# Kernel optimization log

Measured on AMD Instinct MI355X. Metric: run time of the kernel, lower is better.

The kernel has to match this reference:

```python
import jax, jax.numpy as jnp
import numpy as np

B, N, D, H = 4, 4096, 1024, 16
HD = D // H  # 64
EPS_NORM = 1e-12  # F.normalize eps
EPS_LN = 1e-5     # layernorm eps


def setup_inputs() -> dict:
    key = jax.random.key(0)
    ks = jax.random.split(key, 9)
    s = 0.02
    return {
        "x": jax.random.normal(ks[0], (B, N, D), jnp.float32),
        "Wq": jax.random.normal(ks[1], (D, D), jnp.float32) * s,
        "Wk": jax.random.normal(ks[2], (D, D), jnp.float32) * s,
        "Wv": jax.random.normal(ks[3], (D, D), jnp.float32) * s,
        "Wf": jax.random.normal(ks[4], (H, D), jnp.float32) * s,
        "Wg1": jax.random.normal(ks[5], (HD, D), jnp.float32) * s,
        "Wg2": jax.random.normal(ks[6], (D, HD), jnp.float32) * s,
        "ln_w": jnp.ones((D,), jnp.float32),
        "Wo": jax.random.normal(ks[7], (D, D), jnp.float32) * s,
    }


def _silu(x):
    return x * jax.nn.sigmoid(x)


def _simple_gla(q, k, v, f):
    # q,k,v: [B,N,H,HD], f: [B,N,H] log-decay. Recurrence:
    #   S_t = exp(f_t) * S_{t-1} + k_t v_t^T ;  o_t = q_t^T S_t  (scale=1)
    qT = jnp.moveaxis(q, 1, 0)  # [N,B,H,HD]
    kT = jnp.moveaxis(k, 1, 0)
    vT = jnp.moveaxis(v, 1, 0)
    fT = jnp.moveaxis(f, 1, 0)  # [N,B,H]

    def step(S, inp):
        qt, kt, vt, ft = inp
        S = jnp.exp(ft)[..., None, None] * S + kt[..., :, None] * vt[..., None, :]
        o = jnp.einsum('bhk,bhkv->bhv', qt, S)
        return S, o

    S0 = jnp.zeros((q.shape[0], q.shape[2], q.shape[3], v.shape[3]), q.dtype)
    _, o = jax.lax.scan(step, S0, (qT, kT, vT, fT))
    return jnp.moveaxis(o, 0, 1)  # [B,N,H,HD]


def reference(x, Wq, Wk, Wv, Wf, Wg1, Wg2, ln_w, Wo):
    b, n, d = x.shape
    q = _silu(x @ Wq.T).reshape(b, n, H, HD)
    k = _silu(x @ Wk.T).reshape(b, n, H, HD)
    v = _silu(x @ Wv.T).reshape(b, n, H, HD)
    f = jax.nn.log_sigmoid(x @ Wf.T)  # [B,N,H] scalar per-head log decay
    # F.normalize(k, p=2, dim=-1)
    k = k / jnp.maximum(jnp.linalg.norm(k, axis=-1, keepdims=True), EPS_NORM)

    o = _simple_gla(q, k, v, f).reshape(b, n, d)

    # output gate: sigmoid(Linear(d->hd) -> Linear(hd->d))
    gate = jax.nn.sigmoid((x @ Wg1.T) @ Wg2.T)
    o = o * gate

    # layernorm without bias
    mu = jnp.mean(o, axis=-1, keepdims=True)
    xc = o - mu
    var = jnp.mean(xc * xc, axis=-1, keepdims=True)
    o = xc / jnp.sqrt(var + EPS_LN) * ln_w

    return o @ Wo.T
```

## Files before the change

### kernel.cpp

```cpp
#include <hip/hip_runtime.h>
#include <stdint.h>


#define NWIDE 3200

typedef __attribute__((ext_vector_type(4))) float f32x4;
typedef __attribute__((ext_vector_type(4))) unsigned short u16x4;
typedef __attribute__((ext_vector_type(8))) unsigned short u16x8;
typedef __attribute__((ext_vector_type(8))) __bf16 bf16x8;

__device__ __forceinline__ float bf2f(unsigned short u) {
    union { unsigned int i; float f; } c; c.i = ((unsigned int)u) << 16; return c.f;
}
__device__ __forceinline__ unsigned short f2bf(float f) {
    union { float f; unsigned int i; } c; c.f = f;
    return (unsigned short)((c.i + 0x7fffu + ((c.i >> 16) & 1u)) >> 16);
}
__device__ __forceinline__ f32x4 MFMA(bf16x8 a, bf16x8 b, f32x4 c) {
    return __builtin_amdgcn_mfma_f32_16x16x32_bf16(a, b, c, 0, 0, 0);
}
__device__ __forceinline__ void lds16(const void* g, void* l) {
    __builtin_amdgcn_global_load_lds(
        (const __attribute__((address_space(1))) unsigned int*)(uintptr_t)g,
        (__attribute__((address_space(3))) unsigned int*)(unsigned int)(uintptr_t)l,
        16, 0, 0);
}

__global__ __launch_bounds__(256) void k_convert(const float* __restrict__ src,
                                                 unsigned short* __restrict__ dst, int n4) {
    int i = blockIdx.x * 256 + threadIdx.x;
    if (i >= n4) return;
    f32x4 v = ((const f32x4*)src)[i];
    u16x4 o;
#pragma unroll
    for (int e = 0; e < 4; e++) o[e] = f2bf(v[e]);
    ((u16x4*)dst)[i] = o;
}

__global__ __launch_bounds__(256) void k_wcat(const float* __restrict__ Wq, const float* __restrict__ Wk,
                                              const float* __restrict__ Wv, const float* __restrict__ Wf,
                                              const float* __restrict__ Wg1, unsigned short* __restrict__ Wcat) {
    const int r = blockIdx.x, t = threadIdx.x;
    const float* src = nullptr; int sr = r;
    if (r < 1024) { src = Wq; }
    else if (r < 2048) { src = Wk; sr = r - 1024; }
    else if (r < 3072) { src = Wv; sr = r - 2048; }
    else if (r < 3088) { src = Wf; sr = r - 3072; }
    else if (r < 3152) { src = Wg1; sr = r - 3088; }
    u16x4 o;
    if (src) {
        f32x4 v = *(const f32x4*)&src[(size_t)sr * 1024 + 4 * t];
#pragma unroll
        for (int e = 0; e < 4; e++) o[e] = f2bf(v[e]);
    } else {
        o[0] = 0; o[1] = 0; o[2] = 0; o[3] = 0;
    }
    *(u16x4*)&Wcat[(size_t)r * 1024 + 4 * t] = o;
}

template <int MODE>
__global__ __launch_bounds__(256)
void k_gemm(const unsigned short* __restrict__ A, const unsigned short* __restrict__ Bw,
            void* __restrict__ outp, float* __restrict__ zbuf, int M, int N, int K, int ldOut) {
    __shared__ __align__(16) unsigned short As[128 * 32];
    __shared__ __align__(16) unsigned short Bs[128 * 32];
    const int tid = threadIdx.x;
    const int w = tid >> 6, lane = tid & 63;
    const int m0 = blockIdx.x * 128, n0 = blockIdx.y * 128;
    const int srow = lane >> 2, scol = (lane & 3) * 8;
    const int fr = lane & 15, fg = lane >> 4;
    const int wr = w >> 1, wc = w & 1;
    f32x4 acc[4][4] = {};
    const int kc = K >> 5;
    for (int kt = 0; kt < kc; ++kt) {
        const int k0 = kt << 5;
        __syncthreads();
        {
            const unsigned short* ga = A + (size_t)(m0 + 32 * w + srow) * K + k0 + scol;
            lds16(ga, &As[(32 * w) * 32]);
            const unsigned short* ga2 = A + (size_t)(m0 + 32 * w + 16 + srow) * K + k0 + scol;
            lds16(ga2, &As[(32 * w + 16) * 32]);
            const unsigned short* gb = Bw + (size_t)(n0 + 32 * w + srow) * K + k0 + scol;
            lds16(gb, &Bs[(32 * w) * 32]);
            const unsigned short* gb2 = Bw + (size_t)(n0 + 32 * w + 16 + srow) * K + k0 + scol;
            lds16(gb2, &Bs[(32 * w + 16) * 32]);
        }
        __syncthreads();
        bf16x8 av[4], bv[4];
#pragma unroll
        for (int i = 0; i < 4; i++) av[i] = *(const bf16x8*)&As[(64 * wr + 16 * i + fr) * 32 + fg * 8];
#pragma unroll
        for (int j = 0; j < 4; j++) bv[j] = *(const bf16x8*)&Bs[(64 * wc + 16 * j + fr) * 32 + fg * 8];
#pragma unroll
        for (int i = 0; i < 4; i++)
#pragma unroll
            for (int j = 0; j < 4; j++)
                acc[i][j] = MFMA(av[i], bv[j], acc[i][j]);
    }
#pragma unroll
    for (int i = 0; i < 4; i++)
#pragma unroll
        for (int j = 0; j < 4; j++) {
            const int gc = n0 + 64 * wc + 16 * j + fr;
#pragma unroll
            for (int r = 0; r < 4; r++) {
                const int gr = m0 + 64 * wr + 16 * i + 4 * fg + r;
                float v = acc[i][j][r];
                if (MODE == 0) {
                    ((unsigned short*)outp)[(size_t)gr * ldOut + gc] = f2bf(v);
                    if (gc >= 3072 && gc < 3088) zbuf[gr * 16 + (gc - 3072)] = v;
                } else {
                    ((float*)outp)[(size_t)gr * ldOut + gc] = v;
                }
            }
        }
}

__global__ __launch_bounds__(256)
void k_act(unsigned short* __restrict__ Y, const float* __restrict__ zbuf, float* __restrict__ fbuf) {
    const int r = blockIdx.x, t = threadIdx.x;
    unsigned short* Yr = Y + (size_t)r * NWIDE;
    {
        u16x4 a = *(u16x4*)&Yr[4 * t]; u16x4 o;
#pragma unroll
        for (int e = 0; e < 4; e++) { float x = bf2f(a[e]); o[e] = f2bf(x / (1.f + __expf(-x))); }
        *(u16x4*)&Yr[4 * t] = o;
    }
    {
        u16x4 a = *(u16x4*)&Yr[2048 + 4 * t]; u16x4 o;
#pragma unroll
        for (int e = 0; e < 4; e++) { float x = bf2f(a[e]); o[e] = f2bf(x / (1.f + __expf(-x))); }
        *(u16x4*)&Yr[2048 + 4 * t] = o;
    }
    {
        u16x4 a = *(u16x4*)&Yr[1024 + 4 * t];
        float f[4]; float ssum = 0.f;
#pragma unroll
        for (int e = 0; e < 4; e++) { float x = bf2f(a[e]); f[e] = x / (1.f + __expf(-x)); ssum += f[e] * f[e]; }
#pragma unroll
        for (int m = 1; m < 16; m <<= 1) ssum += __shfl_xor(ssum, m, 16);
        float scale = 1.f / fmaxf(sqrtf(ssum), 1e-12f);
        u16x4 o;
#pragma unroll
        for (int e = 0; e < 4; e++) o[e] = f2bf(f[e] * scale);
        *(u16x4*)&Yr[1024 + 4 * t] = o;
    }
    if (t < 16) {
        float z = zbuf[r * 16 + t];
        float f = (z >= 0.f) ? -log1pf(__expf(-z)) : (z - log1pf(__expf(z)));
        fbuf[r * 16 + t] = f;
    }
}

__global__ void k_cumsum(const float* __restrict__ fbuf, float* __restrict__ cbuf) {
    const int cid = blockIdx.x, t = threadIdx.x;
    const int bh = cid >> 6, ic = cid & 63;
    const int b = bh >> 4, h = bh & 15;
    float v = fbuf[(size_t)(b * 4096 + ic * 64 + t) * 16 + h];
#pragma unroll
    for (int off = 1; off < 64; off <<= 1) {
        float u = __shfl_up(v, (unsigned)off, 64);
        if (t >= off) v += u;
    }
    cbuf[(size_t)cid * 64 + t] = v;
}

__global__ __launch_bounds__(256)
void k_chunk_kv(const unsigned short* __restrict__ Y, const float* __restrict__ cbuf,
                unsigned short* __restrict__ St) {
    __shared__ __align__(16) unsigned short Kt[64 * 72];
    __shared__ __align__(16) unsigned short Vt[64 * 72];
    __shared__ float cs[64];
    const int cid = blockIdx.x, tid = threadIdx.x;
    const int bh = cid >> 6, ic = cid & 63;
    const int b = bh >> 4, h = bh & 15;
    if (tid < 64) cs[tid] = cbuf[(size_t)cid * 64 + tid];
    __syncthreads();
    const int s = tid >> 2, c0 = (tid & 3) << 4;
    const float wdec = __expf(cs[63] - cs[s]);
    const size_t rowg = (size_t)(b * 4096 + ic * 64 + s) * NWIDE;
    u16x8 k0v = *(const u16x8*)&Y[rowg + 1024 + h * 64 + c0];
    u16x8 k1v = *(const u16x8*)&Y[rowg + 1024 + h * 64 + c0 + 8];
    u16x8 v0v = *(const u16x8*)&Y[rowg + 2048 + h * 64 + c0];
    u16x8 v1v = *(const u16x8*)&Y[rowg + 2048 + h * 64 + c0 + 8];
#pragma unroll
    for (int e = 0; e < 8; e++) {
        Kt[(c0 + e) * 72 + s] = f2bf(bf2f(k0v[e]) * wdec);
        Kt[(c0 + 8 + e) * 72 + s] = f2bf(bf2f(k1v[e]) * wdec);
        Vt[(c0 + e) * 72 + s] = v0v[e];
        Vt[(c0 + 8 + e) * 72 + s] = v1v[e];
    }
    __syncthreads();
    const int w = tid >> 6, lane = tid & 63;
    const int fr = lane & 15, fg = lane >> 4;
    f32x4 acc[4] = {};
#pragma unroll
    for (int ks = 0; ks < 2; ks++) {
        bf16x8 a = *(const bf16x8*)&Kt[(16 * w + fr) * 72 + ks * 32 + fg * 8];
#pragma unroll
        for (int j = 0; j < 4; j++)
            acc[j] = MFMA(a, *(const bf16x8*)&Vt[(16 * j + fr) * 72 + ks * 32 + fg * 8], acc[j]);
    }
    unsigned short* outp = St + (size_t)cid * 4096;
#pragma unroll
    for (int j = 0; j < 4; j++)
#pragma unroll
        for (int r = 0; r < 4; r++)
            outp[(16 * w + 4 * fg + r) * 64 + 16 * j + fr] = f2bf(acc[j][r]);
}

__global__ void k_scan(unsigned short* __restrict__ St, const float* __restrict__ cbuf) {
    const int bh = blockIdx.x >> 4;
    const int e = ((blockIdx.x & 15) << 8) + threadIdx.x;
    float S = 0.f;
    const size_t base = (size_t)bh * 64 * 4096 + e;
    for (int i = 0; i < 64; i++) {
        const float d = __expf(cbuf[(bh * 64 + i) * 64 + 63]);
        const float m = bf2f(St[base + (size_t)i * 4096]);
        St[base + (size_t)i * 4096] = f2bf(S);
        S = d * S + m;
    }
}

__global__ __launch_bounds__(256)
void k_chunk_out(const unsigned short* __restrict__ Y, const float* __restrict__ cbuf,
                 const unsigned short* __restrict__ St, const unsigned short* __restrict__ Wg2b,
                 unsigned short* __restrict__ og) {
    __shared__ __align__(16) unsigned short Qs[64 * 72];
    __shared__ __align__(16) unsigned short Ks[64 * 72];
    __shared__ __align__(16) unsigned short Vt[64 * 72];
    __shared__ __align__(16) unsigned short S0[64 * 72];
    __shared__ __align__(16) unsigned short G1[64 * 72];
    __shared__ __align__(16) unsigned short W2[64 * 72];
    __shared__ __align__(16) unsigned short Pl[4 * 16 * 72];
    __shared__ float cs[64];
    const int cid = blockIdx.x, tid = threadIdx.x;
    const int bh = cid >> 6, ic = cid & 63;
    const int b = bh >> 4, h = bh & 15;
    if (tid < 64) cs[tid] = cbuf[(size_t)cid * 64 + tid];
    const int s = tid >> 2, c0 = (tid & 3) << 4;
    const size_t rowg = (size_t)(b * 4096 + ic * 64 + s) * NWIDE;
    *(u16x8*)&Qs[s * 72 + c0] = *(const u16x8*)&Y[rowg + h * 64 + c0];
    *(u16x8*)&Qs[s * 72 + c0 + 8] = *(const u16x8*)&Y[rowg + h * 64 + c0 + 8];
    *(u16x8*)&Ks[s * 72 + c0] = *(const u16x8*)&Y[rowg + 1024 + h * 64 + c0];
    *(u16x8*)&Ks[s * 72 + c0 + 8] = *(const u16x8*)&Y[rowg + 1024 + h * 64 + c0 + 8];
    *(u16x8*)&G1[s * 72 + c0] = *(const u16x8*)&Y[rowg + 3088 + c0];
    *(u16x8*)&G1[s * 72 + c0 + 8] = *(const u16x8*)&Y[rowg + 3088 + c0 + 8];
    *(u16x8*)&W2[s * 72 + c0] = *(const u16x8*)&Wg2b[(size_t)(h * 64 + s) * 64 + c0];
    *(u16x8*)&W2[s * 72 + c0 + 8] = *(const u16x8*)&Wg2b[(size_t)(h * 64 + s) * 64 + c0 + 8];
    {
        u16x8 v0v = *(const u16x8*)&Y[rowg + 2048 + h * 64 + c0];
        u16x8 v1v = *(const u16x8*)&Y[rowg + 2048 + h * 64 + c0 + 8];
        u16x8 s0v = *(const u16x8*)&St[(size_t)cid * 4096 + s * 64 + c0];
        u16x8 s1v = *(const u16x8*)&St[(size_t)cid * 4096 + s * 64 + c0 + 8];
#pragma unroll
        for (int e = 0; e < 8; e++) {
            Vt[(c0 + e) * 72 + s] = v0v[e];
            Vt[(c0 + 8 + e) * 72 + s] = v1v[e];
            S0[(c0 + e) * 72 + s] = s0v[e];
            S0[(c0 + 8 + e) * 72 + s] = s1v[e];
        }
    }
    __syncthreads();
    const int w = tid >> 6, lane = tid & 63;
    const int fr = lane & 15, fg = lane >> 4;
    bf16x8 aq[2];
#pragma unroll
    for (int ks = 0; ks < 2; ks++) aq[ks] = *(const bf16x8*)&Qs[(16 * w + fr) * 72 + ks * 32 + fg * 8];
    f32x4 sc[4] = {};
#pragma unroll
    for (int ks = 0; ks < 2; ks++)
#pragma unroll
        for (int j = 0; j < 4; j++)
            sc[j] = MFMA(aq[ks], *(const bf16x8*)&Ks[(16 * j + fr) * 72 + ks * 32 + fg * 8], sc[j]);
    const int tl = 16 * w + 4 * fg;
#pragma unroll
    for (int j = 0; j < 4; j++)
#pragma unroll
        for (int r = 0; r < 4; r++) {
            const int tt = tl + r, ss2 = 16 * j + fr;
            float p = (ss2 <= tt) ? sc[j][r] * __expf(cs[tt] - cs[ss2]) : 0.f;
            Pl[w * (16 * 72) + (4 * fg + r) * 72 + ss2] = f2bf(p);
        }
    __syncthreads();
    f32x4 ov[4] = {};
#pragma unroll
    for (int ks = 0; ks < 2; ks++) {
        bf16x8 ap = *(const bf16x8*)&Pl[w * (16 * 72) + fr * 72 + ks * 32 + fg * 8];
#pragma unroll
        for (int j = 0; j < 4; j++)
            ov[j] = MFMA(ap, *(const bf16x8*)&Vt[(16 * j + fr) * 72 + ks * 32 + fg * 8], ov[j]);
    }
    f32x4 qs[4] = {};
#pragma unroll
    for (int ks = 0; ks < 2; ks++)
#pragma unroll
        for (int j = 0; j < 4; j++)
            qs[j] = MFMA(aq[ks], *(const bf16x8*)&S0[(16 * j + fr) * 72 + ks * 32 + fg * 8], qs[j]);
    bf16x8 ag[2];
#pragma unroll
    for (int ks = 0; ks < 2; ks++) ag[ks] = *(const bf16x8*)&G1[(16 * w + fr) * 72 + ks * 32 + fg * 8];
    f32x4 gl[4] = {};
#pragma unroll
    for (int ks = 0; ks < 2; ks++)
#pragma unroll
        for (int j = 0; j < 4; j++)
            gl[j] = MFMA(ag[ks], *(const bf16x8*)&W2[(16 * j + fr) * 72 + ks * 32 + fg * 8], gl[j]);
#pragma unroll
    for (int j = 0; j < 4; j++)
#pragma unroll
        for (int r = 0; r < 4; r++) {
            const int tt = tl + r;
            const float o = ov[j][r] + __expf(cs[tt]) * qs[j][r];
            const float g = 1.f / (1.f + __expf(-gl[j][r]));
            og[(size_t)(b * 4096 + ic * 64 + tt) * 1024 + h * 64 + 16 * j + fr] = f2bf(o * g);
        }
}

__global__ __launch_bounds__(256)
void k_ln(unsigned short* __restrict__ og, const float* __restrict__ lnw) {
    __shared__ float red[8];
    const int r = blockIdx.x, t = threadIdx.x;
    unsigned short* p = og + (size_t)r * 1024;
    u16x4 a = *(u16x4*)&p[4 * t];
    float x[4]; float s = 0.f, ssum = 0.f;
#pragma unroll
    for (int e = 0; e < 4; e++) { x[e] = bf2f(a[e]); s += x[e]; ssum += x[e] * x[e]; }
#pragma unroll
    for (int m = 1; m < 64; m <<= 1) { s += __shfl_xor(s, m, 64); ssum += __shfl_xor(ssum, m, 64); }
    const int w = t >> 6;
    if ((t & 63) == 0) { red[w] = s; red[4 + w] = ssum; }
    __syncthreads();
    s = red[0] + red[1] + red[2] + red[3];
    ssum = red[4] + red[5] + red[6] + red[7];
    const float mu = s * (1.f / 1024.f);
    const float var = ssum * (1.f / 1024.f) - mu * mu;
    const float rs = rsqrtf(var + 1e-5f);
    u16x4 o;
#pragma unroll
    for (int e = 0; e < 4; e++) o[e] = f2bf((x[e] - mu) * rs * lnw[4 * t + e]);
    *(u16x4*)&p[4 * t] = o;
}

extern "C" void kernel_launch(void* const* d_in, const int* in_sizes, int n_in,
                              void* d_out, int out_size, void* d_ws, size_t ws_size,
                              hipStream_t stream) {
    const float* x = (const float*)d_in[0];
    const float* Wq = (const float*)d_in[1];
    const float* Wk = (const float*)d_in[2];
    const float* Wv = (const float*)d_in[3];
    const float* Wf = (const float*)d_in[4];
    const float* Wg1 = (const float*)d_in[5];
    const float* Wg2 = (const float*)d_in[6];
    const float* lnw = (const float*)d_in[7];
    const float* Wo = (const float*)d_in[8];
    char* ws = (char*)d_ws;
    unsigned short* xb = (unsigned short*)(ws + 0);
    unsigned short* Yb = (unsigned short*)(ws + 33554432LL);
    unsigned short* Wcat = (unsigned short*)(ws + 138412032LL);
    unsigned short* Wob = (unsigned short*)(ws + 144965632LL);
    unsigned short* Wg2b = (unsigned short*)(ws + 147062784LL);
    float* zbuf = (float*)(ws + 147193856LL);
    float* fbuf = (float*)(ws + 148242432LL);
    float* cbuf = (float*)(ws + 149291008LL);
    unsigned short* St = (unsigned short*)(ws + 150339584LL);
    unsigned short* og = (unsigned short*)(ws + 183894016LL);

    k_convert<<<16384, 256, 0, stream>>>(x, xb, 4194304);
    k_wcat<<<3200, 256, 0, stream>>>(Wq, Wk, Wv, Wf, Wg1, Wcat);
    k_convert<<<1024, 256, 0, stream>>>(Wo, Wob, 262144);
    k_convert<<<64, 256, 0, stream>>>(Wg2, Wg2b, 16384);
    k_gemm<0><<<dim3(128, 25), 256, 0, stream>>>(xb, Wcat, Yb, zbuf, 16384, 3200, 1024, 3200);
    k_act<<<16384, 256, 0, stream>>>(Yb, zbuf, fbuf);
    k_cumsum<<<4096, 64, 0, stream>>>(fbuf, cbuf);
    k_chunk_kv<<<4096, 256, 0, stream>>>(Yb, cbuf, St);
    k_scan<<<1024, 256, 0, stream>>>(St, cbuf);
    k_chunk_out<<<4096, 256, 0, stream>>>(Yb, cbuf, St, Wg2b, og);
    k_ln<<<16384, 256, 0, stream>>>(og, lnw);
    k_gemm<1><<<dim3(128, 8), 256, 0, stream>>>(og, Wob, d_out, nullptr, 16384, 1024, 1024, 1024);
}
```

Before: 364.5 us.

## Replace GEMMs with 256x256 double-buffered swizzled kernel and fuse activations into epilogue

```diff
diff --git a/kernel.cpp b/kernel.cpp
--- a/kernel.cpp
+++ b/kernel.cpp
@@ -15,6 +15,10 @@
 __device__ __forceinline__ unsigned short f2bf(float f) {
     union { float f; unsigned int i; } c; c.f = f;
     return (unsigned short)((c.i + 0x7fffu + ((c.i >> 16) & 1u)) >> 16);
+}
+__device__ __forceinline__ float siluf(float x) { return x / (1.f + __expf(-x)); }
+__device__ __forceinline__ float logsigf(float z) {
+    return (z >= 0.f) ? -log1pf(__expf(-z)) : (z - log1pf(__expf(z)));
 }
 __device__ __forceinline__ f32x4 MFMA(bf16x8 a, bf16x8 b, f32x4 c) {
     return __builtin_amdgcn_mfma_f32_16x16x32_bf16(a, b, c, 0, 0, 0);
@@ -58,97 +62,168 @@
     *(u16x4*)&Wcat[(size_t)r * 1024 + 4 * t] = o;
 }
 
+
+template <int I0>
+__device__ __forceinline__ void mfma16(const bf16x8* av, const bf16x8* bv, f32x4 (&acc)[8][4]) {
+#pragma unroll
+    for (int di = 0; di < 2; di++)
+#pragma unroll
+        for (int j = 0; j < 4; j++)
+#pragma unroll
+            for (int ks = 0; ks < 2; ks++)
+                acc[I0 + di][j] = MFMA(av[di * 2 + ks], bv[j * 2 + ks], acc[I0 + di][j]);
+}
+
 template <int MODE>
-__global__ __launch_bounds__(256)
-void k_gemm(const unsigned short* __restrict__ A, const unsigned short* __restrict__ Bw,
-            void* __restrict__ outp, float* __restrict__ zbuf, int M, int N, int K, int ldOut) {
-    __shared__ __align__(16) unsigned short As[128 * 32];
-    __shared__ __align__(16) unsigned short Bs[128 * 32];
+__global__ __launch_bounds__(512, 2)
+void k_gemm256(const unsigned short* __restrict__ A, const unsigned short* __restrict__ Bw,
+               void* __restrict__ outp, float* __restrict__ fbuf, int NT) {
+    __shared__ __align__(16) char smem[131072];
     const int tid = threadIdx.x;
     const int w = tid >> 6, lane = tid & 63;
-    const int m0 = blockIdx.x * 128, n0 = blockIdx.y * 128;
-    const int srow = lane >> 2, scol = (lane & 3) * 8;
     const int fr = lane & 15, fg = lane >> 4;
-    const int wr = w >> 1, wc = w & 1;
-    f32x4 acc[4][4] = {};
-    const int kc = K >> 5;
-    for (int kt = 0; kt < kc; ++kt) {
-        const int k0 = kt << 5;
-        __syncthreads();
-        {
-            const unsigned short* ga = A + (size_t)(m0 + 32 * w + srow) * K + k0 + scol;
-            lds16(ga, &As[(32 * w) * 32]);
-            const unsigned short* ga2 = A + (size_t)(m0 + 32 * w + 16 + srow) * K + k0 + scol;
-            lds16(ga2, &As[(32 * w + 16) * 32]);
-            const unsigned short* gb = Bw + (size_t)(n0 + 32 * w + srow) * K + k0 + scol;
-            lds16(gb, &Bs[(32 * w) * 32]);
-            const unsigned short* gb2 = Bw + (size_t)(n0 + 32 * w + 16 + srow) * K + k0 + scol;
-            lds16(gb2, &Bs[(32 * w + 16) * 32]);
+    const int wr = w >> 2, wc = w & 3;
+    const int swz = (fr & 7) << 4;
+    const int bid = blockIdx.x;
+    const int cpx = gridDim.x >> 3;
+    const int sbid = (bid & 7) * cpx + (bid >> 3);
+    const int mt = sbid / NT, nt = sbid - mt * NT;
+    const int m0 = mt << 8, n0 = nt << 8;
+
+    f32x4 acc[8][4] = {};
+    bf16x8 bv[8];
+
+    auto STAGE = [&](int tile, int half) {
+        const unsigned short* G = (half < 2) ? A : Bw;
+        const int grow0 = ((half < 2) ? m0 : n0) + ((half & 1) << 7);
+        const int dstbase = ((tile & 1) << 16) + (half << 14);
+        const int k0 = tile << 6;
+#pragma unroll
+        for (int q = 0; q < 2; q++) {
+            const int slot = (q << 9) + (w << 6) + lane;
+            const int r = slot >> 3, c = slot & 7;
+            const unsigned short* g = G + (size_t)(grow0 + r) * 1024 + k0 + ((c ^ (r & 7)) << 3);
+            lds16(g, smem + dstbase + (q << 13) + (w << 10));
         }
-        __syncthreads();
-        bf16x8 av[4], bv[4];
-#pragma unroll
-        for (int i = 0; i < 4; i++) av[i] = *(const bf16x8*)&As[(64 * wr + 16 * i + fr) * 32 + fg * 8];
-#pragma unroll
-        for (int j = 0; j < 4; j++) bv[j] = *(const bf16x8*)&Bs[(64 * wc + 16 * j + fr) * 32 + fg * 8];
-#pragma unroll
-        for (int i = 0; i < 4; i++)
+    };
+    auto LDB = [&](int buf) {
+#pragma unroll
+        for (int j = 0; j < 4; j++)
+#pragma unroll
+            for (int ks = 0; ks < 2; ks++) {
+                const int row = (wc << 6) + (j << 4) + fr;
+                const int byt = (buf << 16) + 32768 + (row << 7) + (ks << 6) + (fg << 4);
+                bv[j * 2 + ks] = *(const bf16x8*)(smem + (byt ^ swz));
+            }
+    };
+    auto LDA = [&](int buf, int i0, bf16x8* av) {
+#pragma unroll
+        for (int di = 0; di < 2; di++)
+#pragma unroll
+            for (int ks = 0; ks < 2; ks++) {
+                const int row = (wr << 7) + ((i0 + di) << 4) + fr;
+                const int byt = (buf << 16) + (row << 7) + (ks << 6) + (fg << 4);
+                av[di * 2 + ks] = *(const bf16x8*)(smem + (byt ^ swz));
+            }
+    };
+
+#define GBAR() do { asm volatile("" ::: "memory"); __builtin_amdgcn_s_barrier(); asm volatile("" ::: "memory"); } while (0)
+
+    STAGE(0, 0); STAGE(0, 1); STAGE(0, 2); STAGE(0, 3); STAGE(1, 2); STAGE(1, 3);
+    asm volatile("s_waitcnt vmcnt(4)" ::: "memory");
+    GBAR();
+
+#define PHASE(P, STILE, SHALF)                                              \
+    do {                                                                    \
+        const int tile_ = 2 * t + ((P) >= 4 ? 1 : 0);                       \
+        const int buf_ = tile_ & 1;                                         \
+        bf16x8 av[4];                                                       \
+        if (((P) & 3) == 0) LDB(buf_);                                      \
+        LDA(buf_, 2 * ((P) & 3), av);                                       \
+        const int st_ = 2 * t + (STILE);                                    \
+        if (st_ < 16) STAGE(st_, (SHALF));                                  \
+        GBAR();                                                             \
+        __builtin_amdgcn_s_setprio(1);                                      \
+        mfma16<2 * ((P) & 3)>(av, bv, acc);                                 \
+        __builtin_amdgcn_s_setprio(0);                                      \
+        if (((P) & 3) == 3) asm volatile("s_waitcnt vmcnt(4)" ::: "memory");\
+        GBAR();                                                             \
+    } while (0)
+
+    for (int t = 0; t < 8; t++) {
+        PHASE(0, 1, 0); PHASE(1, 1, 1); PHASE(2, 2, 2); PHASE(3, 2, 3);
+        PHASE(4, 2, 0); PHASE(5, 2, 1); PHASE(6, 3, 2); PHASE(7, 3, 3);
+    }
+#undef PHASE
+#undef GBAR
+
+    const int nb = n0 + (wc << 6);
+    const int rbase = m0 + (wr << 7) + (fg << 2);
+    if (MODE == 1) {
+        float* O = (float*)outp;
+#pragma unroll
+        for (int i = 0; i < 8; i++)
+#pragma unroll
+            for (int j = 0; j < 4; j++) {
+                const int gc = nb + (j << 4) + fr;
+#pragma unroll
+                for (int r = 0; r < 4; r++)
+                    O[(size_t)(rbase + (i << 4) + r) * 1024 + gc] = acc[i][j][r];
+            }
+        return;
+    }
+    unsigned short* Y = (unsigned short*)outp;
+    if (nb >= 3072) {
+#pragma unroll
+        for (int i = 0; i < 8; i++)
+#pragma unroll
+            for (int j = 0; j < 4; j++) {
+                const int gc = nb + (j << 4) + fr;
+#pragma unroll
+                for (int r = 0; r < 4; r++) {
+                    const int gr = rbase + (i << 4) + r;
+                    const float v = acc[i][j][r];
+                    if (gc < 3088) {
+                        if (gc >= 3072) fbuf[gr * 16 + (gc - 3072)] = logsigf(v);
+                    } else if (gc < 3152) {
+                        Y[(size_t)gr * NWIDE + gc] = f2bf(v);
+                    }
+                }
+            }
+    } else if (nb >= 1024 && nb < 2048) {
+#pragma unroll
+        for (int i = 0; i < 8; i++)
 #pragma unroll
             for (int j = 0; j < 4; j++)
-                acc[i][j] = MFMA(av[i], bv[j], acc[i][j]);
-    }
-#pragma unroll
-    for (int i = 0; i < 4; i++)
-#pragma unroll
-        for (int j = 0; j < 4; j++) {
-            const int gc = n0 + 64 * wc + 16 * j + fr;
+#pragma unroll
+                for (int r = 0; r < 4; r++) acc[i][j][r] = siluf(acc[i][j][r]);
+#pragma unroll
+        for (int i = 0; i < 8; i++)
 #pragma unroll
             for (int r = 0; r < 4; r++) {
-                const int gr = m0 + 64 * wr + 16 * i + 4 * fg + r;
-                float v = acc[i][j][r];
-                if (MODE == 0) {
-                    ((unsigned short*)outp)[(size_t)gr * ldOut + gc] = f2bf(v);
-                    if (gc >= 3072 && gc < 3088) zbuf[gr * 16 + (gc - 3072)] = v;
-                } else {
-                    ((float*)outp)[(size_t)gr * ldOut + gc] = v;
-                }
-            }
-        }
-}
-
-__global__ __launch_bounds__(256)
-void k_act(unsigned short* __restrict__ Y, const float* __restrict__ zbuf, float* __restrict__ fbuf) {
-    const int r = blockIdx.x, t = threadIdx.x;
-    unsigned short* Yr = Y + (size_t)r * NWIDE;
-    {
-        u16x4 a = *(u16x4*)&Yr[4 * t]; u16x4 o;
-#pragma unroll
-        for (int e = 0; e < 4; e++) { float x = bf2f(a[e]); o[e] = f2bf(x / (1.f + __expf(-x))); }
-        *(u16x4*)&Yr[4 * t] = o;
-    }
-    {
-        u16x4 a = *(u16x4*)&Yr[2048 + 4 * t]; u16x4 o;
-#pragma unroll
-        for (int e = 0; e < 4; e++) { float x = bf2f(a[e]); o[e] = f2bf(x / (1.f + __expf(-x))); }
-        *(u16x4*)&Yr[2048 + 4 * t] = o;
-    }
-    {
-        u16x4 a = *(u16x4*)&Yr[1024 + 4 * t];
-        float f[4]; float ssum = 0.f;
-#pragma unroll
-        for (int e = 0; e < 4; e++) { float x = bf2f(a[e]); f[e] = x / (1.f + __expf(-x)); ssum += f[e] * f[e]; }
-#pragma unroll
-        for (int m = 1; m < 16; m <<= 1) ssum += __shfl_xor(ssum, m, 16);
-        float scale = 1.f / fmaxf(sqrtf(ssum), 1e-12f);
-        u16x4 o;
-#pragma unroll
-        for (int e = 0; e < 4; e++) o[e] = f2bf(f[e] * scale);
-        *(u16x4*)&Yr[1024 + 4 * t] = o;
-    }
-    if (t < 16) {
-        float z = zbuf[r * 16 + t];
-        float f = (z >= 0.f) ? -log1pf(__expf(-z)) : (z - log1pf(__expf(z)));
-        fbuf[r * 16 + t] = f;
+                float ss = 0.f;
+#pragma unroll
+                for (int j = 0; j < 4; j++) ss += acc[i][j][r] * acc[i][j][r];
+                ss += __shfl_xor(ss, 1, 64);
+                ss += __shfl_xor(ss, 2, 64);
+                ss += __shfl_xor(ss, 4, 64);
+                ss += __shfl_xor(ss, 8, 64);
+                const float sc = 1.f / fmaxf(sqrtf(ss), 1e-12f);
+                const int gr = rbase + (i << 4) + r;
+#pragma unroll
+                for (int j = 0; j < 4; j++)
+                    Y[(size_t)gr * NWIDE + nb + (j << 4) + fr] = f2bf(acc[i][j][r] * sc);
+            }
+    } else {
+#pragma unroll
+        for (int i = 0; i < 8; i++)
+#pragma unroll
+            for (int j = 0; j < 4; j++) {
+                const int gc = nb + (j << 4) + fr;
+#pragma unroll
+                for (int r = 0; r < 4; r++)
+                    Y[(size_t)(rbase + (i << 4) + r) * NWIDE + gc] = f2bf(siluf(acc[i][j][r]));
+            }
     }
 }
 
@@ -358,24 +433,22 @@
     unsigned short* xb = (unsigned short*)(ws + 0);
     unsigned short* Yb = (unsigned short*)(ws + 33554432LL);
     unsigned short* Wcat = (unsigned short*)(ws + 138412032LL);
-    unsigned short* Wob = (unsigned short*)(ws + 144965632LL);
-    unsigned short* Wg2b = (unsigned short*)(ws + 147062784LL);
-    float* zbuf = (float*)(ws + 147193856LL);
-    float* fbuf = (float*)(ws + 148242432LL);
-    float* cbuf = (float*)(ws + 149291008LL);
-    unsigned short* St = (unsigned short*)(ws + 150339584LL);
-    unsigned short* og = (unsigned short*)(ws + 183894016LL);
+    unsigned short* Wob = (unsigned short*)(ws + 145227776LL);
+    unsigned short* Wg2b = (unsigned short*)(ws + 147324928LL);
+    float* fbuf = (float*)(ws + 147456000LL);
+    float* cbuf = (float*)(ws + 148504576LL);
+    unsigned short* St = (unsigned short*)(ws + 149553152LL);
+    unsigned short* og = xb;
 
     k_convert<<<16384, 256, 0, stream>>>(x, xb, 4194304);
-    k_wcat<<<3200, 256, 0, stream>>>(Wq, Wk, Wv, Wf, Wg1, Wcat);
+    k_wcat<<<3328, 256, 0, stream>>>(Wq, Wk, Wv, Wf, Wg1, Wcat);
     k_convert<<<1024, 256, 0, stream>>>(Wo, Wob, 262144);
     k_convert<<<64, 256, 0, stream>>>(Wg2, Wg2b, 16384);
-    k_gemm<0><<<dim3(128, 25), 256, 0, stream>>>(xb, Wcat, Yb, zbuf, 16384, 3200, 1024, 3200);
-    k_act<<<16384, 256, 0, stream>>>(Yb, zbuf, fbuf);
+    k_gemm256<0><<<832, 512, 0, stream>>>(xb, Wcat, Yb, fbuf, 13);
     k_cumsum<<<4096, 64, 0, stream>>>(fbuf, cbuf);
     k_chunk_kv<<<4096, 256, 0, stream>>>(Yb, cbuf, St);
     k_scan<<<1024, 256, 0, stream>>>(St, cbuf);
     k_chunk_out<<<4096, 256, 0, stream>>>(Yb, cbuf, St, Wg2b, og);
     k_ln<<<16384, 256, 0, stream>>>(og, lnw);
-    k_gemm<1><<<dim3(128, 8), 256, 0, stream>>>(og, Wob, d_out, nullptr, 16384, 1024, 1024, 1024);
-}
+    k_gemm256<1><<<256, 512, 0, stream>>>(og, Wob, d_out, nullptr, 4);
+}
```

After: 388.5 us. 1.07x slower.

## Fuse SiLU, key L2-norm and log-sigmoid into projection GEMM epilogue

Applied to the files above, without the earlier changes.

```diff
diff --git a/kernel.cpp b/kernel.cpp
--- a/kernel.cpp
+++ b/kernel.cpp
@@ -15,6 +15,10 @@
 __device__ __forceinline__ unsigned short f2bf(float f) {
     union { float f; unsigned int i; } c; c.f = f;
     return (unsigned short)((c.i + 0x7fffu + ((c.i >> 16) & 1u)) >> 16);
+}
+__device__ __forceinline__ float siluf(float x) { return x / (1.f + __expf(-x)); }
+__device__ __forceinline__ float logsigf(float z) {
+    return (z >= 0.f) ? -log1pf(__expf(-z)) : (z - log1pf(__expf(z)));
 }
 __device__ __forceinline__ f32x4 MFMA(bf16x8 a, bf16x8 b, f32x4 c) {
     return __builtin_amdgcn_mfma_f32_16x16x32_bf16(a, b, c, 0, 0, 0);
@@ -61,12 +65,14 @@
 template <int MODE>
 __global__ __launch_bounds__(256)
 void k_gemm(const unsigned short* __restrict__ A, const unsigned short* __restrict__ Bw,
-            void* __restrict__ outp, float* __restrict__ zbuf, int M, int N, int K, int ldOut) {
+            void* __restrict__ outp, float* __restrict__ fbuf, int M, int N, int K, int ldOut) {
     __shared__ __align__(16) unsigned short As[128 * 32];
     __shared__ __align__(16) unsigned short Bs[128 * 32];
     const int tid = threadIdx.x;
     const int w = tid >> 6, lane = tid & 63;
-    const int m0 = blockIdx.x * 128, n0 = blockIdx.y * 128;
+    const int cpx = gridDim.x >> 3;
+    const int mt = (blockIdx.x & 7) * cpx + (blockIdx.x >> 3);
+    const int m0 = mt * 128, n0 = blockIdx.y * 128;
     const int srow = lane >> 2, scol = (lane & 3) * 8;
     const int fr = lane & 15, fg = lane >> 4;
     const int wr = w >> 1, wc = w & 1;
@@ -97,58 +103,72 @@
             for (int j = 0; j < 4; j++)
                 acc[i][j] = MFMA(av[i], bv[j], acc[i][j]);
     }
-#pragma unroll
-    for (int i = 0; i < 4; i++)
-#pragma unroll
-        for (int j = 0; j < 4; j++) {
-            const int gc = n0 + 64 * wc + 16 * j + fr;
-#pragma unroll
-            for (int r = 0; r < 4; r++) {
-                const int gr = m0 + 64 * wr + 16 * i + 4 * fg + r;
-                float v = acc[i][j][r];
-                if (MODE == 0) {
-                    ((unsigned short*)outp)[(size_t)gr * ldOut + gc] = f2bf(v);
-                    if (gc >= 3072 && gc < 3088) zbuf[gr * 16 + (gc - 3072)] = v;
-                } else {
-                    ((float*)outp)[(size_t)gr * ldOut + gc] = v;
+    const int nb = n0 + 64 * wc;
+    if (MODE == 1) {
+        float* O = (float*)outp;
+#pragma unroll
+        for (int i = 0; i < 4; i++)
+#pragma unroll
+            for (int j = 0; j < 4; j++) {
+                const int gc = nb + 16 * j + fr;
+#pragma unroll
+                for (int r = 0; r < 4; r++)
+                    O[(size_t)(m0 + 64 * wr + 16 * i + 4 * fg + r) * ldOut + gc] = acc[i][j][r];
+            }
+        return;
+    }
+    unsigned short* Y = (unsigned short*)outp;
+    if (nb >= 3072) {
+#pragma unroll
+        for (int i = 0; i < 4; i++)
+#pragma unroll
+            for (int j = 0; j < 4; j++) {
+                const int gc = nb + 16 * j + fr;
+#pragma unroll
+                for (int r = 0; r < 4; r++) {
+                    const int gr = m0 + 64 * wr + 16 * i + 4 * fg + r;
+                    const float v = acc[i][j][r];
+                    if (gc < 3088) {
+                        if (gc >= 3072) fbuf[gr * 16 + (gc - 3072)] = logsigf(v);
+                    } else if (gc < 3152) {
+                        Y[(size_t)gr * ldOut + gc] = f2bf(v);
+                    }
                 }
             }
-        }
-}
-
-__global__ __launch_bounds__(256)
-void k_act(unsigned short* __restrict__ Y, const float* __restrict__ zbuf, float* __restrict__ fbuf) {
-    const int r = blockIdx.x, t = threadIdx.x;
-    unsigned short* Yr = Y + (size_t)r * NWIDE;
-    {
-        u16x4 a = *(u16x4*)&Yr[4 * t]; u16x4 o;
-#pragma unroll
-        for (int e = 0; e < 4; e++) { float x = bf2f(a[e]); o[e] = f2bf(x / (1.f + __expf(-x))); }
-        *(u16x4*)&Yr[4 * t] = o;
-    }
-    {
-        u16x4 a = *(u16x4*)&Yr[2048 + 4 * t]; u16x4 o;
-#pragma unroll
-        for (int e = 0; e < 4; e++) { float x = bf2f(a[e]); o[e] = f2bf(x / (1.f + __expf(-x))); }
-        *(u16x4*)&Yr[2048 + 4 * t] = o;
-    }
-    {
-        u16x4 a = *(u16x4*)&Yr[1024 + 4 * t];
-        float f[4]; float ssum = 0.f;
-#pragma unroll
-        for (int e = 0; e < 4; e++) { float x = bf2f(a[e]); f[e] = x / (1.f + __expf(-x)); ssum += f[e] * f[e]; }
-#pragma unroll
-        for (int m = 1; m < 16; m <<= 1) ssum += __shfl_xor(ssum, m, 16);
-        float scale = 1.f / fmaxf(sqrtf(ssum), 1e-12f);
-        u16x4 o;
-#pragma unroll
-        for (int e = 0; e < 4; e++) o[e] = f2bf(f[e] * scale);
-        *(u16x4*)&Yr[1024 + 4 * t] = o;
-    }
-    if (t < 16) {
-        float z = zbuf[r * 16 + t];
-        float f = (z >= 0.f) ? -log1pf(__expf(-z)) : (z - log1pf(__expf(z)));
-        fbuf[r * 16 + t] = f;
+    } else if (nb >= 1024 && nb < 2048) {
+#pragma unroll
+        for (int i = 0; i < 4; i++)
+#pragma unroll
+            for (int j = 0; j < 4; j++)
+#pragma unroll
+                for (int r = 0; r < 4; r++) acc[i][j][r] = siluf(acc[i][j][r]);
+#pragma unroll
+        for (int i = 0; i < 4; i++)
+#pragma unroll
+            for (int r = 0; r < 4; r++) {
+                float ss = 0.f;
+#pragma unroll
+                for (int j = 0; j < 4; j++) ss += acc[i][j][r] * acc[i][j][r];
+                ss += __shfl_xor(ss, 1, 64);
+                ss += __shfl_xor(ss, 2, 64);
+                ss += __shfl_xor(ss, 4, 64);
+                ss += __shfl_xor(ss, 8, 64);
+                const float sc = 1.f / fmaxf(sqrtf(ss), 1e-12f);
+                const int gr = m0 + 64 * wr + 16 * i + 4 * fg + r;
+#pragma unroll
+                for (int j = 0; j < 4; j++)
+                    Y[(size_t)gr * ldOut + nb + 16 * j + fr] = f2bf(acc[i][j][r] * sc);
+            }
+    } else {
+#pragma unroll
+        for (int i = 0; i < 4; i++)
+#pragma unroll
+            for (int j = 0; j < 4; j++) {
+                const int gc = nb + 16 * j + fr;
+#pragma unroll
+                for (int r = 0; r < 4; r++)
+                    Y[(size_t)(m0 + 64 * wr + 16 * i + 4 * fg + r) * ldOut + gc] = f2bf(siluf(acc[i][j][r]));
+            }
     }
 }
 
@@ -360,18 +380,16 @@
     unsigned short* Wcat = (unsigned short*)(ws + 138412032LL);
     unsigned short* Wob = (unsigned short*)(ws + 144965632LL);
     unsigned short* Wg2b = (unsigned short*)(ws + 147062784LL);
-    float* zbuf = (float*)(ws + 147193856LL);
-    float* fbuf = (float*)(ws + 148242432LL);
-    float* cbuf = (float*)(ws + 149291008LL);
-    unsigned short* St = (unsigned short*)(ws + 150339584LL);
-    unsigned short* og = (unsigned short*)(ws + 183894016LL);
+    float* fbuf = (float*)(ws + 147193856LL);
+    float* cbuf = (float*)(ws + 148242432LL);
+    unsigned short* St = (unsigned short*)(ws + 149291008LL);
+    unsigned short* og = xb;
 
     k_convert<<<16384, 256, 0, stream>>>(x, xb, 4194304);
     k_wcat<<<3200, 256, 0, stream>>>(Wq, Wk, Wv, Wf, Wg1, Wcat);
     k_convert<<<1024, 256, 0, stream>>>(Wo, Wob, 262144);
     k_convert<<<64, 256, 0, stream>>>(Wg2, Wg2b, 16384);
-    k_gemm<0><<<dim3(128, 25), 256, 0, stream>>>(xb, Wcat, Yb, zbuf, 16384, 3200, 1024, 3200);
-    k_act<<<16384, 256, 0, stream>>>(Yb, zbuf, fbuf);
+    k_gemm<0><<<dim3(128, 25), 256, 0, stream>>>(xb, Wcat, Yb, fbuf, 16384, 3200, 1024, 3200);
     k_cumsum<<<4096, 64, 0, stream>>>(fbuf, cbuf);
     k_chunk_kv<<<4096, 256, 0, stream>>>(Yb, cbuf, St);
     k_scan<<<1024, 256, 0, stream>>>(St, cbuf);
```

Result: faster. 355.8 us (-2.4%).
